# Kernel tuning notes

Measured on AMD Instinct MI355X. Metric: run time of the kernel, lower is better.

The kernel has to match this reference:

```python
import jax, jax.numpy as jnp
import numpy as np

NU = 100000  # num user nodes
NI = 100000  # num item nodes
E = 1600000  # edges per edge type
L = 100000   # labeled edges
H = 128      # hidden_channels
EPS = 1e-12  # F.normalize eps


def sage_conv(x_src, x_dst, edge_index, w_l, b_l, w_r, num_dst):
    """PyG SAGEConv, mean aggregation, normalize=True.
    w_l, w_r: [H, H] stored as [in, out]; lin_r has no bias."""
    src, dst = edge_index[0], edge_index[1]
    msg_sum = jax.ops.segment_sum(x_src[src], dst, num_segments=num_dst)  # [num_dst, H]
    cnt = jax.ops.segment_sum(jnp.ones((src.shape[0],), x_src.dtype), dst, num_segments=num_dst)
    mean = msg_sum / jnp.maximum(cnt, 1.0)[:, None]
    out = mean @ w_l + b_l + x_dst @ w_r
    norm = jnp.sqrt(jnp.sum(out * out, axis=-1, keepdims=True))
    return out / jnp.maximum(norm, EPS)


def setup_inputs() -> dict:
    key = jax.random.key(0)
    ks = jax.random.split(key, 20)
    s = 1.0 / np.sqrt(H)
    d = {
        'emb_user': jax.random.normal(ks[0], (NU, H), jnp.float32),
        'emb_item': jax.random.normal(ks[1], (NI, H), jnp.float32),
        'edge_rates': jax.random.randint(ks[2], (2, E), 0, 100000, jnp.int32),
        'edge_rev': jax.random.randint(ks[3], (2, E), 0, 100000, jnp.int32),
        'edge_label_index': jax.random.randint(ks[4], (2, L), 0, 100000, jnp.int32),
    }
    names = ['w1l_rates', 'w1r_rates', 'w1l_rev', 'w1r_rev',
             'w2l_rates', 'w2r_rates', 'w2l_rev', 'w2r_rev']
    for i, n in enumerate(names):
        d[n] = jax.random.uniform(ks[5 + i], (H, H), jnp.float32, -s, s)
    for i, n in enumerate(['b1_rates', 'b1_rev', 'b2_rates', 'b2_rev']):
        d[n] = jax.random.uniform(ks[13 + i], (H,), jnp.float32, -s, s)
    return d


def reference(emb_user, emb_item, edge_rates, edge_rev, edge_label_index,
              w1l_rates, w1r_rates, w1l_rev, w1r_rev,
              w2l_rates, w2r_rates, w2l_rev, w2r_rev,
              b1_rates, b1_rev, b2_rates, b2_rev):
    xu, xi = emb_user, emb_item
    # layer 1: each node type receives exactly one edge type (HeteroConv mean is identity)
    xi1 = sage_conv(xu, xi, edge_rates, w1l_rates, b1_rates, w1r_rates, NI)
    xu1 = sage_conv(xi, xu, edge_rev, w1l_rev, b1_rev, w1r_rev, NU)
    xu1 = jax.nn.relu(xu1)  # dropout is identity in eval mode
    xi1 = jax.nn.relu(xi1)
    # layer 2
    xi2 = sage_conv(xu1, xi1, edge_rates, w2l_rates, b2_rates, w2r_rates, NI)
    xu2 = sage_conv(xi1, xu1, edge_rev, w2l_rev, b2_rev, w2r_rev, NU)
    xu2 = jax.nn.relu(xu2)
    xi2 = jax.nn.relu(xi2)
    # classifier: dot(user[src], item[dst])
    x_src = xu2[edge_label_index[0]]
    x_dst = xi2[edge_label_index[1]]
    return jnp.sum(x_src * x_dst, axis=-1)
```

## Files before the change

### kernel.cpp

```cpp
#include <hip/hip_runtime.h>
#include <hip/hip_bf16.h>

#define NUM_U 100000
#define NUM_I 100000
#define NE    1600000
#define NL    100000
#define CAP   48
#define NBIN  391
#define BINCAP 4608
#define ROUND  4096
#define PB    391

typedef __attribute__((ext_vector_type(4))) float floatx4;
typedef __attribute__((ext_vector_type(8))) short shortx8;
typedef unsigned long long u64;

__device__ __forceinline__ float bf_lo(unsigned v) { return __uint_as_float(v << 16); }
__device__ __forceinline__ float bf_hi(unsigned v) { return __uint_as_float(v & 0xffff0000u); }

__device__ __forceinline__ unsigned pack_bf16x2(float lo, float hi) {
    __hip_bfloat16 l = __float2bfloat16(lo);
    __hip_bfloat16 h = __float2bfloat16(hi);
    unsigned short ul = *(unsigned short*)&l;
    unsigned short uh = *(unsigned short*)&h;
    return (unsigned)ul | ((unsigned)uh << 16);
}

__device__ __forceinline__ int clampi(int x, int hi) {
    return min(max(x, 0), hi - 1);
}

__global__ void zero_f32_kernel(float* __restrict__ p, int n) {
    int i = blockIdx.x * blockDim.x + threadIdx.x;
    if (i < n) p[i] = 0.0f;
}

__global__ void conv2_kernel(const float* __restrict__ emb_u, const float* __restrict__ emb_i,
                             unsigned* __restrict__ xu, unsigned* __restrict__ xi) {
    int i = blockIdx.x * blockDim.x + threadIdx.x;
    const int nu = NUM_U * 64;
    if (i < nu) {
        float2 v = ((const float2*)emb_u)[i];
        xu[i] = pack_bf16x2(v.x, v.y);
    } else if (i < nu + NUM_I * 64) {
        int j = i - nu;
        float2 v = ((const float2*)emb_i)[j];
        xi[j] = pack_bf16x2(v.x, v.y);
    }
}

__global__ void transpose_w4_kernel(
    const float* __restrict__ w1l_rates, const float* __restrict__ w1r_rates,
    const float* __restrict__ w1l_rev,   const float* __restrict__ w1r_rev,
    const float* __restrict__ w2l_rates, const float* __restrict__ w2r_rates,
    const float* __restrict__ w2l_rev,   const float* __restrict__ w2r_rev,
    short* __restrict__ Bt, int* __restrict__ bin_cursor) {
    int idx = blockIdx.x * blockDim.x + threadIdx.x;
    if (idx < 2 * NBIN) bin_cursor[idx] = 0;
    int which = idx >> 15;
    int r = idx & 32767;
    int n = r >> 8;
    int k = r & 255;
    const float *wl, *wr;
    switch (which) {
        case 0:  wl = w1l_rates; wr = w1r_rates; break;
        case 1:  wl = w1l_rev;   wr = w1r_rev;   break;
        case 2:  wl = w2l_rates; wr = w2r_rates; break;
        default: wl = w2l_rev;   wr = w2r_rev;   break;
    }
    float v = (k < 128) ? wl[k * 128 + n] : wr[(k - 128) * 128 + n];
    __hip_bfloat16 b = __float2bfloat16(v);
    Bt[idx] = *(const short*)&b;
}

__global__ __launch_bounds__(256) void partition2_kernel(
    const int* __restrict__ edges0, const int* __restrict__ edges1,
    u64* __restrict__ bd0, u64* __restrict__ bd1, int* __restrict__ cur) {
    __shared__ int hist[NBIN];
    __shared__ int prefix[NBIN];
    __shared__ int gbase[NBIN];
    __shared__ __align__(16) u64 sorted[ROUND];

    const int type = (blockIdx.x >= PB) ? 1 : 0;
    const int* edges = type ? edges1 : edges0;
    u64* bin_data = type ? bd1 : bd0;
    int* bin_cursor = cur + type * NBIN;
    const int blk  = blockIdx.x - type * PB;
    const int tid  = threadIdx.x;
    const int lane = tid & 63;
    const int wv   = tid >> 6;
    const int base = blk * ROUND;

    for (int k = tid; k < NBIN; k += 256) hist[k] = 0;
    __syncthreads();

    int mybin[16], myrank[16], mysrc[16], mydst[16];
#pragma unroll
    for (int r = 0; r < 16; r++) {
        int i = base + r * 256 + tid;
        mybin[r] = -1;
        if (i < NE) {
            mysrc[r] = clampi(edges[i], NUM_U);
            mydst[r] = clampi(edges[i + NE], NUM_I);
            mybin[r] = mydst[r] >> 8;
            myrank[r] = atomicAdd(&hist[mybin[r]], 1);
        }
    }
    __syncthreads();

    if (wv == 0) {
        int carry = 0;
        for (int c = 0; c < NBIN; c += 64) {
            int idx = c + lane;
            int h = (idx < NBIN) ? hist[idx] : 0;
            int v = h;
            for (int o = 1; o < 64; o <<= 1) {
                int t = __shfl_up(v, o);
                if (lane >= o) v += t;
            }
            if (idx < NBIN) prefix[idx] = v - h + carry;
            carry += __shfl(v, 63);
        }
    }
    __syncthreads();

#pragma unroll
    for (int r = 0; r < 16; r++) {
        if (mybin[r] >= 0) {
            int j = prefix[mybin[r]] + myrank[r];
            sorted[j] = ((u64)(unsigned)mydst[r] << 32) | (unsigned)mysrc[r];
        }
    }
    __syncthreads();

    for (int b = tid; b < NBIN; b += 256) {
        int cnt = hist[b];
        gbase[b] = (cnt > 0) ? atomicAdd(&bin_cursor[b], cnt) : 0;
    }
    __syncthreads();

    int total = min(ROUND, NE - base);
    for (int j = tid; j < total; j += 256) {
        u64 e = sorted[j];
        int b = (int)(e >> 40);
        int pos = gbase[b] + (j - prefix[b]);
        if (pos < BINCAP)
            bin_data[(size_t)b * BINCAP + pos] = e;
    }
}

__global__ __launch_bounds__(256) void binscatter2_kernel(
    const u64* __restrict__ bd0, const u64* __restrict__ bd1, const int* __restrict__ cur,
    int* __restrict__ deg0, int* __restrict__ bucket0,
    int* __restrict__ deg1, int* __restrict__ bucket1) {
    __shared__ int lbucket[256 * CAP];
    __shared__ int ldeg[256];
    const int type = (blockIdx.x >= NBIN) ? 1 : 0;
    const int b = blockIdx.x - type * NBIN;
    const u64* bin_data = type ? bd1 : bd0;
    int* deg = type ? deg1 : deg0;
    int* bucket = type ? bucket1 : bucket0;
    const int tid = threadIdx.x;
    const int dstbase = b << 8;
    const int n_dst = NUM_I;

    ldeg[tid] = 0;
    __syncthreads();

    int count = min(cur[type * NBIN + b], BINCAP);
    for (int j = tid; j < count; j += 256) {
        u64 e = bin_data[(size_t)b * BINCAP + j];
        int src = (int)(unsigned)e;
        int dl = ((int)(e >> 32)) & 255;
        int pos = atomicAdd(&ldeg[dl], 1);
        if (pos < CAP) lbucket[dl * CAP + pos] = src;
    }
    __syncthreads();

    if (dstbase + tid < n_dst) deg[dstbase + tid] = ldeg[tid];
    int limit = min(256, n_dst - dstbase) * CAP;
    for (int k = tid; k < limit; k += 256)
        bucket[(size_t)dstbase * CAP + k] = lbucket[k];
}

__global__ __launch_bounds__(256) void agg2_kernel(
    const int* __restrict__ degA, const int* __restrict__ bucketA,
    const unsigned* __restrict__ xA, unsigned* __restrict__ outA,
    const int* __restrict__ degB, const int* __restrict__ bucketB,
    const unsigned* __restrict__ xB, unsigned* __restrict__ outB) {
    const int bid = blockIdx.x;
    const int xcd = bid & 7;
    const int typeB = (xcd >= 4);
    const int gidx = (bid >> 3) * 4 + (xcd & 3);
    const int node = gidx * 4 + (threadIdx.x >> 6);
    const int lane = threadIdx.x & 63;
    if (node >= NUM_I) return;

    const int* deg; const int* bucket; const unsigned* xb; unsigned* mo;
    if (!typeB) { deg = degA; bucket = bucketA; xb = xA; mo = outA; }
    else        { deg = degB; bucket = bucketB; xb = xB; mo = outB; }

    int d = __builtin_nontemporal_load(&deg[node]);
    int cnt = min(d, CAP);
    int srcs = (lane < cnt) ? __builtin_nontemporal_load(&bucket[(size_t)node * CAP + lane]) : 0;
    float a0 = 0.f, a1 = 0.f;
    int e = 0;
    for (; e + 8 <= cnt; e += 8) {
        int s0 = __builtin_amdgcn_readlane(srcs, e + 0);
        int s1 = __builtin_amdgcn_readlane(srcs, e + 1);
        int s2 = __builtin_amdgcn_readlane(srcs, e + 2);
        int s3 = __builtin_amdgcn_readlane(srcs, e + 3);
        int s4 = __builtin_amdgcn_readlane(srcs, e + 4);
        int s5 = __builtin_amdgcn_readlane(srcs, e + 5);
        int s6 = __builtin_amdgcn_readlane(srcs, e + 6);
        int s7 = __builtin_amdgcn_readlane(srcs, e + 7);
        unsigned v0 = xb[(size_t)s0 * 64 + lane];
        unsigned v1 = xb[(size_t)s1 * 64 + lane];
        unsigned v2 = xb[(size_t)s2 * 64 + lane];
        unsigned v3 = xb[(size_t)s3 * 64 + lane];
        unsigned v4 = xb[(size_t)s4 * 64 + lane];
        unsigned v5 = xb[(size_t)s5 * 64 + lane];
        unsigned v6 = xb[(size_t)s6 * 64 + lane];
        unsigned v7 = xb[(size_t)s7 * 64 + lane];
        a0 += bf_lo(v0) + bf_lo(v1) + bf_lo(v2) + bf_lo(v3)
            + bf_lo(v4) + bf_lo(v5) + bf_lo(v6) + bf_lo(v7);
        a1 += bf_hi(v0) + bf_hi(v1) + bf_hi(v2) + bf_hi(v3)
            + bf_hi(v4) + bf_hi(v5) + bf_hi(v6) + bf_hi(v7);
    }
    for (; e + 4 <= cnt; e += 4) {
        int s0 = __builtin_amdgcn_readlane(srcs, e + 0);
        int s1 = __builtin_amdgcn_readlane(srcs, e + 1);
        int s2 = __builtin_amdgcn_readlane(srcs, e + 2);
        int s3 = __builtin_amdgcn_readlane(srcs, e + 3);
        unsigned v0 = xb[(size_t)s0 * 64 + lane];
        unsigned v1 = xb[(size_t)s1 * 64 + lane];
        unsigned v2 = xb[(size_t)s2 * 64 + lane];
        unsigned v3 = xb[(size_t)s3 * 64 + lane];
        a0 += bf_lo(v0) + bf_lo(v1) + bf_lo(v2) + bf_lo(v3);
        a1 += bf_hi(v0) + bf_hi(v1) + bf_hi(v2) + bf_hi(v3);
    }
    for (; e < cnt; e++) {
        int s0 = __builtin_amdgcn_readlane(srcs, e);
        unsigned v0 = xb[(size_t)s0 * 64 + lane];
        a0 += bf_lo(v0); a1 += bf_hi(v0);
    }
    float scale = 1.0f / (float)max(d, 1);
    __builtin_nontemporal_store(pack_bf16x2(a0 * scale, a1 * scale),
                                &mo[(size_t)node * 64 + lane]);
}

__global__ __launch_bounds__(256) void gemm2_kernel(
    const unsigned* __restrict__ meanA, unsigned* __restrict__ xA,
    const short* __restrict__ BtA, const float* __restrict__ biasA,
    const unsigned* __restrict__ meanB, unsigned* __restrict__ xB,
    const short* __restrict__ BtB, const float* __restrict__ biasB,
    int nblocksA) {
    __shared__ __align__(16) short A_lds[128 * 72];
    __shared__ float rowsum[128][2];

    const int half = (blockIdx.x >= nblocksA) ? 1 : 0;
    const unsigned* meanb = half ? meanB : meanA;
    const unsigned* xdstb = half ? xB : xA;
    unsigned* outb = half ? xB : xA;
    const short* Bt = half ? BtB : BtA;
    const float* bias = half ? biasB : biasA;
    const int rb = (blockIdx.x - half * nblocksA) * 128;
    const int n_rows = NUM_I;

    const int tid  = threadIdx.x;
    const int lane = tid & 63;
    const int wv   = tid >> 6;
    const int wm   = wv >> 1;
    const int wn   = wv & 1;
    const int l15  = lane & 15;
    const int lq   = lane >> 4;

    floatx4 acc[4][4];
#pragma unroll
    for (int nt = 0; nt < 4; nt++) {
        float b = bias[wn * 64 + nt * 16 + l15];
#pragma unroll
        for (int mt = 0; mt < 4; mt++) acc[mt][nt] = (floatx4){b, b, b, b};
    }

    for (int kt = 0; kt < 4; kt++) {
        __syncthreads();
        const unsigned* srcbuf = (kt < 2) ? meanb : xdstb;
        const int kbase_u = (kt & 1) * 32;
#pragma unroll
        for (int j = 0; j < 4; j++) {
            int c = tid + j * 256;
            int row = c >> 3;
            int kc = (c & 7) * 8;
            int grow = rb + row;
            uint4 v = make_uint4(0u, 0u, 0u, 0u);
            if (grow < n_rows)
                v = *(const uint4*)(srcbuf + (size_t)grow * 64 + kbase_u + (kc >> 1));
            *(uint4*)&A_lds[row * 72 + kc] = v;
        }
        __syncthreads();

#pragma unroll
        for (int kk = 0; kk < 64; kk += 32) {
            shortx8 af[4], bfr[4];
#pragma unroll
            for (int mt = 0; mt < 4; mt++) {
                int row_l = wm * 64 + mt * 16 + l15;
                af[mt] = *(const shortx8*)&A_lds[row_l * 72 + kk + lq * 8];
            }
#pragma unroll
            for (int nt = 0; nt < 4; nt++) {
                int col = wn * 64 + nt * 16 + l15;
                int kg = kt * 64 + kk + lq * 8;
                bfr[nt] = *(const shortx8*)(Bt + col * 256 + kg);
            }
#pragma unroll
            for (int mt = 0; mt < 4; mt++)
#pragma unroll
                for (int nt = 0; nt < 4; nt++)
                    acc[mt][nt] = __builtin_amdgcn_mfma_f32_16x16x32_bf16(
                        af[mt], bfr[nt], acc[mt][nt], 0, 0, 0);
        }
    }

#pragma unroll
    for (int mt = 0; mt < 4; mt++) {
#pragma unroll
        for (int r = 0; r < 4; r++) {
            float p = 0.f;
#pragma unroll
            for (int nt = 0; nt < 4; nt++) { float x = acc[mt][nt][r]; p += x * x; }
            for (int o = 1; o < 16; o <<= 1) p += __shfl_xor(p, o);
            if (l15 == 0) rowsum[wm * 64 + mt * 16 + lq * 4 + r][wn] = p;
        }
    }
    __syncthreads();

#pragma unroll
    for (int mt = 0; mt < 4; mt++) {
#pragma unroll
        for (int r = 0; r < 4; r++) {
            int row_l = wm * 64 + mt * 16 + lq * 4 + r;
            int grow = rb + row_l;
            float s = rowsum[row_l][0] + rowsum[row_l][1];
            float inv = 1.f / fmaxf(sqrtf(s), 1e-12f);
#pragma unroll
            for (int nt = 0; nt < 4; nt++) {
                float v = fmaxf(acc[mt][nt][r] * inv, 0.f);
                float vnb = __shfl_xor(v, 1);
                if (grow < n_rows && (l15 & 1) == 0) {
                    int colpair = (wn * 64 + nt * 16 + l15) >> 1;
                    outb[(size_t)grow * 64 + colpair] = pack_bf16x2(v, vnb);
                }
            }
        }
    }
}

__global__ __launch_bounds__(256) void classifier_kernel(
    const unsigned* __restrict__ xu, const unsigned* __restrict__ xi,
    const int* __restrict__ eli, float* __restrict__ out, int nL) {
    int wave = (blockIdx.x * blockDim.x + threadIdx.x) >> 6;
    int lane = threadIdx.x & 63;
    if (wave >= nL) return;
    int su = clampi(eli[wave], NUM_U);
    int di = clampi(eli[wave + nL], NUM_I);
    unsigned a = xu[(size_t)su * 64 + lane];
    unsigned b = xi[(size_t)di * 64 + lane];
    float p = bf_lo(a) * bf_lo(b) + bf_hi(a) * bf_hi(b);
    for (int o = 32; o; o >>= 1) p += __shfl_xor(p, o);
    if (lane == 0) __builtin_nontemporal_store(p, &out[wave]);
}

extern "C" void kernel_launch(void* const* d_in, const int* in_sizes, int n_in,
                              void* d_out, int out_size, void* d_ws, size_t ws_size,
                              hipStream_t stream) {
    const float* emb_user = (const float*)d_in[0];
    const float* emb_item = (const float*)d_in[1];
    const int* edge_rates = (const int*)d_in[2];
    const int* edge_rev   = (const int*)d_in[3];
    const int* eli        = (const int*)d_in[4];
    const float* b1_rates = (const float*)d_in[13];
    const float* b1_rev   = (const float*)d_in[14];
    const float* b2_rates = (const float*)d_in[15];
    const float* b2_rev   = (const float*)d_in[16];

    char* p = (char*)d_ws;
    auto alloc = [&](size_t bytes) -> void* {
        void* q = (void*)p;
        p += (bytes + 511) & ~(size_t)511;
        return q;
    };
    int* deg_rates    = (int*)alloc((size_t)NUM_I * 4);
    int* bucket_rates = (int*)alloc((size_t)NUM_I * CAP * 4);
    int* deg_rev      = (int*)alloc((size_t)NUM_U * 4);
    int* bucket_rev   = (int*)alloc((size_t)NUM_U * CAP * 4);
    unsigned* meanI = (unsigned*)alloc((size_t)NUM_I * 64 * 4);
    unsigned* meanU = (unsigned*)alloc((size_t)NUM_U * 64 * 4);
    unsigned* xi    = (unsigned*)alloc((size_t)NUM_I * 64 * 4);
    unsigned* xu    = (unsigned*)alloc((size_t)NUM_U * 64 * 4);
    short* Bt = (short*)alloc((size_t)4 * 32768 * 2);
    int* bin_cursor = (int*)alloc((size_t)2 * NBIN * 4);
    u64* bd0 = (u64*)meanI;
    u64* bd1 = (u64*)meanU;

    const int gemmBlocks = (NUM_I + 127) / 128;
    const int agg2Blocks = 2 * ((NUM_I + 3) / 4);
    const int conv2Blocks = ((NUM_U + NUM_I) * 64 + 255) / 256;

    if (out_size > NL) {
        int tail = out_size - NL;
        zero_f32_kernel<<<(tail + 255) / 256, 256, 0, stream>>>((float*)d_out + NL, tail);
    }

    transpose_w4_kernel<<<512, 256, 0, stream>>>(
        (const float*)d_in[5], (const float*)d_in[6],
        (const float*)d_in[7], (const float*)d_in[8],
        (const float*)d_in[9], (const float*)d_in[10],
        (const float*)d_in[11], (const float*)d_in[12], Bt, bin_cursor);
    conv2_kernel<<<conv2Blocks, 256, 0, stream>>>(emb_user, emb_item, xu, xi);
    partition2_kernel<<<2 * PB, 256, 0, stream>>>(edge_rates, edge_rev, bd0, bd1, bin_cursor);
    binscatter2_kernel<<<2 * NBIN, 256, 0, stream>>>(bd0, bd1, bin_cursor,
                                                     deg_rates, bucket_rates,
                                                     deg_rev, bucket_rev);

    agg2_kernel<<<agg2Blocks, 256, 0, stream>>>(deg_rates, bucket_rates, xu, meanI,
                                                deg_rev, bucket_rev, xi, meanU);
    gemm2_kernel<<<2 * gemmBlocks, 256, 0, stream>>>(meanI, xi, Bt + 0 * 32768, b1_rates,
                                                     meanU, xu, Bt + 1 * 32768, b1_rev,
                                                     gemmBlocks);

    agg2_kernel<<<agg2Blocks, 256, 0, stream>>>(deg_rates, bucket_rates, xu, meanI,
                                                deg_rev, bucket_rev, xi, meanU);
    gemm2_kernel<<<2 * gemmBlocks, 256, 0, stream>>>(meanI, xi, Bt + 2 * 32768, b2_rates,
                                                     meanU, xu, Bt + 3 * 32768, b2_rev,
                                                     gemmBlocks);

    classifier_kernel<<<(NL * 64 + 255) / 256, 256, 0, stream>>>(xu, xi, eli,
                                                                 (float*)d_out, NL);
}
```

Before: 631.6 us.

## Merge prep kernels into fewer launches and load GEMM A fragments directly

The tail zeroing is folded into the weight-transpose kernel, and the bf16 embedding conversion is folded into the partition kernel as extra blocks, cutting two kernel launches. The GEMM no longer stages the A tile through LDS with two barriers per k-step. Each wave now loads its MFMA A fragments straight from global memory into registers. This removes LDS traffic and syncs, but it means more uncoalesced 16-byte global loads, and rows are reloaded by the two wn waves.

```diff
diff --git a/kernel.cpp b/kernel.cpp
--- a/kernel.cpp
+++ b/kernel.cpp
@@ -13,6 +13,7 @@
 
 typedef __attribute__((ext_vector_type(4))) float floatx4;
 typedef __attribute__((ext_vector_type(8))) short shortx8;
+typedef __attribute__((ext_vector_type(4))) unsigned uintx4;
 typedef unsigned long long u64;
 
 __device__ __forceinline__ float bf_lo(unsigned v) { return __uint_as_float(v << 16); }
@@ -30,56 +31,59 @@
     return min(max(x, 0), hi - 1);
 }
 
-__global__ void zero_f32_kernel(float* __restrict__ p, int n) {
-    int i = blockIdx.x * blockDim.x + threadIdx.x;
-    if (i < n) p[i] = 0.0f;
-}
-
-__global__ void conv2_kernel(const float* __restrict__ emb_u, const float* __restrict__ emb_i,
-                             unsigned* __restrict__ xu, unsigned* __restrict__ xi) {
-    int i = blockIdx.x * blockDim.x + threadIdx.x;
-    const int nu = NUM_U * 64;
-    if (i < nu) {
-        float2 v = ((const float2*)emb_u)[i];
-        xu[i] = pack_bf16x2(v.x, v.y);
-    } else if (i < nu + NUM_I * 64) {
-        int j = i - nu;
-        float2 v = ((const float2*)emb_i)[j];
-        xi[j] = pack_bf16x2(v.x, v.y);
-    }
-}
-
-__global__ void transpose_w4_kernel(
+__global__ void prep1_kernel(
     const float* __restrict__ w1l_rates, const float* __restrict__ w1r_rates,
     const float* __restrict__ w1l_rev,   const float* __restrict__ w1r_rev,
     const float* __restrict__ w2l_rates, const float* __restrict__ w2r_rates,
     const float* __restrict__ w2l_rev,   const float* __restrict__ w2r_rev,
-    short* __restrict__ Bt, int* __restrict__ bin_cursor) {
+    short* __restrict__ Bt, int* __restrict__ bin_cursor,
+    float* __restrict__ tailp, int ntail) {
     int idx = blockIdx.x * blockDim.x + threadIdx.x;
     if (idx < 2 * NBIN) bin_cursor[idx] = 0;
-    int which = idx >> 15;
-    int r = idx & 32767;
-    int n = r >> 8;
-    int k = r & 255;
-    const float *wl, *wr;
-    switch (which) {
-        case 0:  wl = w1l_rates; wr = w1r_rates; break;
-        case 1:  wl = w1l_rev;   wr = w1r_rev;   break;
-        case 2:  wl = w2l_rates; wr = w2r_rates; break;
-        default: wl = w2l_rev;   wr = w2r_rev;   break;
-    }
-    float v = (k < 128) ? wl[k * 128 + n] : wr[(k - 128) * 128 + n];
-    __hip_bfloat16 b = __float2bfloat16(v);
-    Bt[idx] = *(const short*)&b;
-}
-
-__global__ __launch_bounds__(256) void partition2_kernel(
+    if (idx < 4 * 32768) {
+        int which = idx >> 15;
+        int r = idx & 32767;
+        int n = r >> 8;
+        int k = r & 255;
+        const float *wl, *wr;
+        switch (which) {
+            case 0:  wl = w1l_rates; wr = w1r_rates; break;
+            case 1:  wl = w1l_rev;   wr = w1r_rev;   break;
+            case 2:  wl = w2l_rates; wr = w2r_rates; break;
+            default: wl = w2l_rev;   wr = w2r_rev;   break;
+        }
+        float v = (k < 128) ? wl[k * 128 + n] : wr[(k - 128) * 128 + n];
+        __hip_bfloat16 b = __float2bfloat16(v);
+        Bt[idx] = *(const short*)&b;
+    } else {
+        int t = idx - 4 * 32768;
+        if (t < ntail) tailp[t] = 0.0f;
+    }
+}
+
+__global__ __launch_bounds__(256) void prep2_kernel(
     const int* __restrict__ edges0, const int* __restrict__ edges1,
-    u64* __restrict__ bd0, u64* __restrict__ bd1, int* __restrict__ cur) {
+    u64* __restrict__ bd0, u64* __restrict__ bd1, int* __restrict__ cur,
+    const float* __restrict__ emb_u, const float* __restrict__ emb_i,
+    unsigned* __restrict__ xu, unsigned* __restrict__ xi) {
     __shared__ int hist[NBIN];
     __shared__ int prefix[NBIN];
     __shared__ int gbase[NBIN];
     __shared__ __align__(16) u64 sorted[ROUND];
+
+    if (blockIdx.x >= 2 * PB) {
+        int i = (blockIdx.x - 2 * PB) * blockDim.x + threadIdx.x;
+        const int nu = NUM_U * 64;
+        if (i < nu) {
+            float2 v = ((const float2*)emb_u)[i];
+            xu[i] = pack_bf16x2(v.x, v.y);
+        } else if (i < nu + NUM_I * 64) {
+            int j = i - nu;
+            float2 v = ((const float2*)emb_i)[j];
+            xi[j] = pack_bf16x2(v.x, v.y);
+        }
+        return;
+    }
 
     const int type = (blockIdx.x >= PB) ? 1 : 0;
     const int* edges = type ? edges1 : edges0;
@@ -189,9 +193,9 @@
     const int* __restrict__ degB, const int* __restrict__ bucketB,
     const unsigned* __restrict__ xB, unsigned* __restrict__ outB) {
     const int bid = blockIdx.x;
-    const int xcd = bid & 7;
-    const int typeB = (xcd >= 4);
-    const int gidx = (bid >> 3) * 4 + (xcd & 3);
+    const int g = bid & 7;
+    const int typeB = (g >= 4);
+    const int gidx = (bid >> 3) * 4 + (g & 3);
     const int node = gidx * 4 + (threadIdx.x >> 6);
     const int lane = threadIdx.x & 63;
     if (node >= NUM_I) return;
@@ -249,13 +253,12 @@
                                 &mo[(size_t)node * 64 + lane]);
 }
 
-__global__ __launch_bounds__(256) void gemm2_kernel(
+__global__ __launch_bounds__(256) void gemm2r_kernel(
     const unsigned* __restrict__ meanA, unsigned* __restrict__ xA,
     const short* __restrict__ BtA, const float* __restrict__ biasA,
     const unsigned* __restrict__ meanB, unsigned* __restrict__ xB,
     const short* __restrict__ BtB, const float* __restrict__ biasB,
     int nblocksA) {
-    __shared__ __align__(16) short A_lds[128 * 72];
     __shared__ float rowsum[128][2];
 
     const int half = (blockIdx.x >= nblocksA) ? 1 : 0;
@@ -284,34 +287,27 @@
     }
 
     for (int kt = 0; kt < 4; kt++) {
-        __syncthreads();
         const unsigned* srcbuf = (kt < 2) ? meanb : xdstb;
         const int kbase_u = (kt & 1) * 32;
-#pragma unroll
-        for (int j = 0; j < 4; j++) {
-            int c = tid + j * 256;
-            int row = c >> 3;
-            int kc = (c & 7) * 8;
-            int grow = rb + row;
-            uint4 v = make_uint4(0u, 0u, 0u, 0u);
-            if (grow < n_rows)
-                v = *(const uint4*)(srcbuf + (size_t)grow * 64 + kbase_u + (kc >> 1));
-            *(uint4*)&A_lds[row * 72 + kc] = v;
-        }
-        __syncthreads();
-
-#pragma unroll
-        for (int kk = 0; kk < 64; kk += 32) {
-            shortx8 af[4], bfr[4];
-#pragma unroll
-            for (int mt = 0; mt < 4; mt++) {
-                int row_l = wm * 64 + mt * 16 + l15;
-                af[mt] = *(const shortx8*)&A_lds[row_l * 72 + kk + lq * 8];
+        uintx4 a8[4][2];
+#pragma unroll
+        for (int mt = 0; mt < 4; mt++) {
+#pragma unroll
+            for (int kk2 = 0; kk2 < 2; kk2++) {
+                int grow = rb + wm * 64 + mt * 16 + l15;
+                uintx4 v = (uintx4){0u, 0u, 0u, 0u};
+                if (grow < n_rows)
+                    v = *(const uintx4*)(srcbuf + (size_t)grow * 64 + kbase_u + kk2 * 16 + lq * 4);
+                a8[mt][kk2] = v;
             }
+        }
+#pragma unroll
+        for (int kk2 = 0; kk2 < 2; kk2++) {
+            shortx8 bfr[4];
 #pragma unroll
             for (int nt = 0; nt < 4; nt++) {
                 int col = wn * 64 + nt * 16 + l15;
-                int kg = kt * 64 + kk + lq * 8;
+                int kg = kt * 64 + kk2 * 32 + lq * 8;
                 bfr[nt] = *(const shortx8*)(Bt + col * 256 + kg);
             }
 #pragma unroll
@@ -319,7 +315,7 @@
 #pragma unroll
                 for (int nt = 0; nt < 4; nt++)
                     acc[mt][nt] = __builtin_amdgcn_mfma_f32_16x16x32_bf16(
-                        af[mt], bfr[nt], acc[mt][nt], 0, 0, 0);
+                        *(const shortx8*)&a8[mt][kk2], bfr[nt], acc[mt][nt], 0, 0, 0);
         }
     }
 
@@ -408,33 +404,33 @@
     const int agg2Blocks = 2 * ((NUM_I + 3) / 4);
     const int conv2Blocks = ((NUM_U + NUM_I) * 64 + 255) / 256;
 
-    if (out_size > NL) {
-        int tail = out_size - NL;
-        zero_f32_kernel<<<(tail + 255) / 256, 256, 0, stream>>>((float*)d_out + NL, tail);
-    }
-
-    transpose_w4_kernel<<<512, 256, 0, stream>>>(
+    const int ntail = (out_size > NL) ? (out_size - NL) : 0;
+    const int prep1Blocks = 512 + (ntail + 255) / 256;
+    const int prep2Blocks = 2 * PB + conv2Blocks;
+
+    prep1_kernel<<<prep1Blocks, 256, 0, stream>>>(
         (const float*)d_in[5], (const float*)d_in[6],
         (const float*)d_in[7], (const float*)d_in[8],
         (const float*)d_in[9], (const float*)d_in[10],
-        (const float*)d_in[11], (const float*)d_in[12], Bt, bin_cursor);
-    conv2_kernel<<<conv2Blocks, 256, 0, stream>>>(emb_user, emb_item, xu, xi);
-    partition2_kernel<<<2 * PB, 256, 0, stream>>>(edge_rates, edge_rev, bd0, bd1, bin_cursor);
+        (const float*)d_in[11], (const float*)d_in[12], Bt, bin_cursor,
+        (float*)d_out + NL, ntail);
+    prep2_kernel<<<prep2Blocks, 256, 0, stream>>>(edge_rates, edge_rev, bd0, bd1, bin_cursor,
+                                                  emb_user, emb_item, xu, xi);
     binscatter2_kernel<<<2 * NBIN, 256, 0, stream>>>(bd0, bd1, bin_cursor,
                                                      deg_rates, bucket_rates,
                                                      deg_rev, bucket_rev);
 
     agg2_kernel<<<agg2Blocks, 256, 0, stream>>>(deg_rates, bucket_rates, xu, meanI,
                                                 deg_rev, bucket_rev, xi, meanU);
-    gemm2_kernel<<<2 * gemmBlocks, 256, 0, stream>>>(meanI, xi, Bt + 0 * 32768, b1_rates,
-                                                     meanU, xu, Bt + 1 * 32768, b1_rev,
-                                                     gemmBlocks);
+    gemm2r_kernel<<<2 * gemmBlocks, 256, 0, stream>>>(meanI, xi, Bt + 0 * 32768, b1_rates,
+                                                      meanU, xu, Bt + 1 * 32768, b1_rev,
+                                                      gemmBlocks);
 
     agg2_kernel<<<agg2Blocks, 256, 0, stream>>>(deg_rates, bucket_rates, xu, meanI,
                                                 deg_rev, bucket_rev, xi, meanU);
-    gemm2_kernel<<<2 * gemmBlocks, 256, 0, stream>>>(meanI, xi, Bt + 2 * 32768, b2_rates,
-                                                     meanU, xu, Bt + 3 * 32768, b2_rev,
-                                                     gemmBlocks);
+    gemm2r_kernel<<<2 * gemmBlocks, 256, 0, stream>>>(meanI, xi, Bt + 2 * 32768, b2_rates,
+                                                      meanU, xu, Bt + 3 * 32768, b2_rev,
+                                                      gemmBlocks);
 
     classifier_kernel<<<(NL * 64 + 255) / 256, 256, 0, stream>>>(xu, xi, eli,
                                                                  (float*)d_out, NL);
```

Result: no change. 638.1 us (+1.0%).
